# Kernel tuning notes

Measured on AMD Instinct MI355X. Metric: run time of the kernel, lower is better.

The kernel has to match this reference:

```python
import jax, jax.numpy as jnp
import numpy as np

N, S, E = 50000, 16, 400000
D, EDIM = 128, 64
H, K = 4, 32          # n_head, per-head output_dim
NMP, DEPTH = 2, 2


def attn_agg(x, neigh, Wq, Wk, Wv):
    # x: [n, D], neigh: [n, s, D], W*: [H, D, K]
    q = jnp.einsum('nd,hdk->nhk', x, Wq)
    k = jnp.einsum('nsd,hdk->nshk', neigh, Wk)
    v = jnp.einsum('nsd,hdk->nshk', neigh, Wv)
    scale = jnp.asarray(1.0 / np.sqrt(K), x.dtype)
    scores = jnp.einsum('nhk,nshk->nhs', q, k) * scale
    attn = jax.nn.softmax(scores, axis=-1)
    out = jax.nn.elu(jnp.einsum('nhs,nshk->nhk', attn, v))  # activation per head
    return out.reshape(out.shape[0], H * K)                  # concat heads


def setup_inputs():
    key = jax.random.key(0)
    ks = jax.random.split(key, 14)
    sD, sE = 1.0 / np.sqrt(D), 1.0 / np.sqrt(EDIM)
    return {
        'feats': jax.random.normal(ks[0], (N, D), jnp.float32),
        'node_emb': jax.random.normal(ks[1], (N, D), jnp.float32) * 0.02,
        'Wprep': jax.random.normal(ks[2], (D, D), jnp.float32) * sD,
        'edge_emb': jax.random.normal(ks[3], (NMP, E, EDIM), jnp.float32),
        'Wedgeprep': jax.random.normal(ks[4], (NMP, EDIM, D), jnp.float32) * sE,
        'Wq_e': jax.random.normal(ks[5], (NMP, DEPTH, H, D, K), jnp.float32) * sD,
        'Wk_e': jax.random.normal(ks[6], (NMP, DEPTH, H, D, K), jnp.float32) * sD,
        'Wv_e': jax.random.normal(ks[7], (NMP, DEPTH, H, D, K), jnp.float32) * sD,
        'Wq_n': jax.random.normal(ks[8], (NMP, DEPTH, H, D, K), jnp.float32) * sD,
        'Wk_n': jax.random.normal(ks[9], (NMP, DEPTH, H, D, K), jnp.float32) * sD,
        'Wv_n': jax.random.normal(ks[10], (NMP, DEPTH, H, D, K), jnp.float32) * sD,
        'node2edge_idx': jax.random.randint(ks[11], (NMP, N, S), 0, E, jnp.int32),
        'edge_node_adj': jax.random.randint(ks[12], (NMP, E, 2), 0, N, jnp.int32),
    }


def reference(feats, node_emb, Wprep, edge_emb, Wedgeprep,
              Wq_e, Wk_e, Wv_e, Wq_n, Wk_n, Wv_n,
              node2edge_idx, edge_node_adj):
    outputs = []
    for mp in range(NMP):
        f = jax.lax.stop_gradient(feats)           # feats[all_ids].detach()
        dummy_feats = node_emb                      # prep layer_idx=0 (id embedding)
        all_feats = f @ Wprep                       # prep layer_idx=1
        all_edges = edge_emb[mp] @ Wedgeprep[mp]    # edge_prep[mp], shuffle=False
        skip = []
        for l in range(DEPTH):
            # --- edge update: gather 2 endpoint node feats per edge ---
            en = all_feats[edge_node_adj[mp]]       # [E, 2, D]
            next_edges = attn_agg(all_edges, en, Wq_e[mp, l], Wk_e[mp, l], Wv_e[mp, l])
            # --- node update: gather S incident edge feats per node (OLD edges) ---
            x = dummy_feats if l == 0 else all_feats
            ne = all_edges[node2edge_idx[mp]]       # [N, S, D]
            next_feats = attn_agg(x, ne, Wq_n[mp, l], Wk_n[mp, l], Wv_n[mp, l])
            skip.append(next_feats)
            all_feats, all_edges = next_feats, next_edges
        outputs.append(jnp.concatenate(skip, axis=-1))  # [N, DEPTH*H*K]
    return jnp.stack(outputs, axis=0)                   # [NMP, N, DEPTH*H*K]
```

## Files before the change

### kernel.cpp

```cpp
#include <hip/hip_runtime.h>

#define N_NODES 50000
#define S_NEI 16
#define E_EDGES 400000
#define DDIM 128
#define EDIMC 64
#define NMPC 2
#define DEPTHC 2

typedef __attribute__((ext_vector_type(8))) short short8v;
typedef __attribute__((ext_vector_type(4))) float float4v;

__device__ __forceinline__ unsigned short f2bf(float f) {
  unsigned int u = __float_as_uint(f);
  unsigned int r = (u + 0x7fffu + ((u >> 16) & 1u)) >> 16;
  return (unsigned short)r;
}
__device__ __forceinline__ float bf2f(unsigned short h) { return __uint_as_float((unsigned int)h << 16); }
__device__ __forceinline__ float bfs(short h) { return bf2f((unsigned short)h); }
__device__ __forceinline__ float elu_fast(float x) { return x > 0.f ? x : (__expf(x) - 1.0f); }

__global__ void build_wt(const float* __restrict__ Wprep, const float* __restrict__ Wedgeprep,
                         const float* __restrict__ Wq_e, const float* __restrict__ Wk_e,
                         const float* __restrict__ Wv_e, const float* __restrict__ Wq_n,
                         const float* __restrict__ Wk_n, const float* __restrict__ Wv_n,
                         unsigned short* __restrict__ WT) {
  int idx = blockIdx.x * 256 + threadIdx.x;
  if (idx >= 27 * 16384) return;
  int slot = idx >> 14, r = idx & 16383;
  float v = 0.f;
  if (slot < 24) {
    int ml = slot / 6, mat = slot % 6;
    int c = r >> 7, d = r & 127;
    int h = c >> 5, kk = c & 31;
    const float* W = (mat == 0) ? Wk_e : (mat == 1) ? Wv_e : (mat == 2) ? Wq_n
                   : (mat == 3) ? Wq_e : (mat == 4) ? Wk_n : Wv_n;
    v = W[(((size_t)ml * 4 + h) * 128 + d) * 32 + kk];
  } else if (slot == 24) {
    int c = r >> 7, d = r & 127;
    v = Wprep[d * 128 + c];
  } else {
    int mp = slot - 25;
    int c = r >> 6, k = r & 63;
    if (c < 128) v = Wedgeprep[((size_t)mp * 64 + k) * 128 + c];
  }
  WT[idx] = f2bf(v);
}

__global__ void build_qk(const float* __restrict__ Wq_n, const float* __restrict__ Wk_n,
                         unsigned short* __restrict__ QT) {
  int idx = blockIdx.x * 256 + threadIdx.x;
  int mh = idx >> 14, r = idx & 16383;
  int cp = r >> 7, d = r & 127;
  const float* q = Wq_n + ((size_t)mh * 128 + d) * 32;
  const float* k = Wk_n + ((size_t)mh * 128 + cp) * 32;
  float s = 0.f;
  #pragma unroll
  for (int j = 0; j < 32; ++j) s += q[j] * k[j];
  QT[idx] = f2bf(s);
}

__global__ void build_wv(const float* __restrict__ Wv_n, unsigned short* __restrict__ WV) {
  int idx = blockIdx.x * 256 + threadIdx.x;
  int ml = idx >> 14, r14 = idx & 16383;
  int r = r14 >> 7, d = r14 & 127;
  int h = r >> 5, kp = r & 31;
  WV[idx] = f2bf(Wv_n[(((size_t)ml * 4 + h) * 128 + d) * 32 + kp]);
}

template<int KDIM, int NW, bool ASPLIT>
__global__ __launch_bounds__(256, 3)
void proj(const unsigned short* __restrict__ Xbf, const float* __restrict__ Xf,
          const unsigned short* __restrict__ WT,
          unsigned short* __restrict__ Y0, unsigned short* __restrict__ Y1,
          unsigned short* __restrict__ Y2, unsigned short* __restrict__ Y3,
          int rs0, int rs1, int rs2, int rs3, int M) {
  constexpr int NKK  = KDIM / 32;
  constexpr int CHPR = KDIM / 8;
  constexpr int SWZ  = CHPR - 1;
  __shared__ unsigned short Wl[128 * KDIM];
  const int tid  = threadIdx.x;
  const int lane = tid & 63;
  const int wv   = tid >> 6;
  const int l15  = lane & 15, lg = lane >> 4;
  const long m0  = (long)blockIdx.x * 128 + wv * 32;

  short8v xb[2][NKK];
  #pragma unroll
  for (int rf = 0; rf < 2; ++rf) {
    long row = m0 + rf * 16 + l15; if (row >= M) row = M - 1;
    #pragma unroll
    for (int kk = 0; kk < NKK; ++kk) {
      const int k0 = kk * 32 + lg * 8;
      if (ASPLIT) {
        const float* p = Xf + row * KDIM + k0;
        float4v a0 = *(const float4v*)p;
        float4v a1 = *(const float4v*)(p + 4);
        #pragma unroll
        for (int j = 0; j < 8; ++j) {
          float x = (j < 4) ? a0[j] : a1[j - 4];
          xb[rf][kk][j] = (short)f2bf(x);
        }
      } else {
        xb[rf][kk] = *(const short8v*)(Xbf + row * KDIM + k0);
      }
    }
  }

  unsigned short* Ys[4] = {Y0, Y1, Y2, Y3};
  const int rsv[4] = {rs0, rs1, rs2, rs3};
  #pragma unroll
  for (int w = 0; w < NW; ++w) {
    if (w) __syncthreads();
    {
      const uint4* src = (const uint4*)(WT + (size_t)w * 16384);
      #pragma unroll
      for (int i = 0; i < CHPR / 2; ++i) {
        int ci = i * 256 + tid;
        int row = ci / CHPR, ch = ci & SWZ;
        uint4 v = src[ci];
        *(uint4*)((char*)Wl + row * (KDIM * 2) + ((ch ^ (row & SWZ)) << 4)) = v;
      }
    }
    __syncthreads();

    float4v acc[8][2];
    #pragma unroll
    for (int cf = 0; cf < 8; ++cf)
      #pragma unroll
      for (int rf = 0; rf < 2; ++rf) acc[cf][rf] = (float4v)0.f;

    #pragma unroll
    for (int kk = 0; kk < NKK; ++kk) {
      #pragma unroll
      for (int cf = 0; cf < 8; ++cf) {
        const int row = cf * 16 + l15;
        const int ch  = (kk * 4 + lg) ^ (row & SWZ);
        short8v b = *(const short8v*)((char*)Wl + row * (KDIM * 2) + (ch << 4));
        acc[cf][0] = __builtin_amdgcn_mfma_f32_16x16x32_bf16(b, xb[0][kk], acc[cf][0], 0, 0, 0);
        acc[cf][1] = __builtin_amdgcn_mfma_f32_16x16x32_bf16(b, xb[1][kk], acc[cf][1], 0, 0, 0);
      }
    }

    #pragma unroll
    for (int rf = 0; rf < 2; ++rf) {
      const long m = m0 + rf * 16 + l15;
      if (m < M) {
        #pragma unroll
        for (int cf = 0; cf < 8; ++cf) {
          const int c0 = cf * 16 + lg * 4;
          float4v a = acc[cf][rf];
          ushort4 o;
          o.x = f2bf(a[0]); o.y = f2bf(a[1]); o.z = f2bf(a[2]); o.w = f2bf(a[3]);
          *(ushort4*)(Ys[w] + m * (long)rsv[w] + c0) = o;
        }
      }
    }
  }
}

template<int PREP>
__global__ __launch_bounds__(512, 4)
void edge_fused(unsigned short* __restrict__ eold, const unsigned short* __restrict__ WTq,
                const unsigned short* __restrict__ KVn, const int* __restrict__ adj,
                unsigned short* __restrict__ enew,
                const float* __restrict__ emb, const unsigned short* __restrict__ WTprep) {
  __shared__ unsigned short Wl[128 * 128];
  const int tid  = threadIdx.x;
  const int lane = tid & 63;
  const int wv   = tid >> 6;
  const int l15  = lane & 15, lg = lane >> 4;
  const long m0  = (long)blockIdx.x * 128 + wv * 16;

  const long e = m0 + l15;
  const int2 nn = *(const int2*)(adj + e * 2);
  const size_t b0 = (size_t)nn.x * 256, b1 = (size_t)nn.y * 256;

  ushort4 gk0[8], gk1[8], gv0[8], gv1[8];
  if (!PREP) {
    #pragma unroll
    for (int cf = 0; cf < 8; ++cf) {
      const int c0 = cf * 16 + lg * 4;
      gk0[cf] = *(const ushort4*)(KVn + b0 + c0);
      gk1[cf] = *(const ushort4*)(KVn + b1 + c0);
      gv0[cf] = *(const ushort4*)(KVn + b0 + 128 + c0);
      gv1[cf] = *(const ushort4*)(KVn + b1 + 128 + c0);
    }
  }

  short8v xb[4];
  if (PREP) {
    {
      const uint4* src = (const uint4*)WTprep;
      #pragma unroll
      for (int i = 0; i < 2; ++i) {
        int ci = i * 512 + tid;
        int row = ci >> 3, ch = ci & 7;
        uint4 v = src[ci];
        *(uint4*)((char*)Wl + row * 128 + ((ch ^ (row & 7)) << 4)) = v;
      }
    }
    short8v eb[2];
    {
      const long row = m0 + l15;
      #pragma unroll
      for (int kk = 0; kk < 2; ++kk) {
        const float* p = emb + row * 64 + kk * 32 + lg * 8;
        float4v a0 = *(const float4v*)p;
        float4v a1 = *(const float4v*)(p + 4);
        #pragma unroll
        for (int j = 0; j < 8; ++j) {
          float x = (j < 4) ? a0[j] : a1[j - 4];
          eb[kk][j] = (short)f2bf(x);
        }
      }
    }
    __syncthreads();
    float4v accP[8];
    #pragma unroll
    for (int cf = 0; cf < 8; ++cf) accP[cf] = (float4v)0.f;
    #pragma unroll
    for (int kk = 0; kk < 2; ++kk) {
      #pragma unroll
      for (int cf = 0; cf < 8; ++cf) {
        const int row = cf * 16 + l15;
        const int ch  = (kk * 4 + lg) ^ (row & 7);
        short8v b = *(const short8v*)((char*)Wl + row * 128 + (ch << 4));
        accP[cf] = __builtin_amdgcn_mfma_f32_16x16x32_bf16(b, eb[kk], accP[cf], 0, 0, 0);
      }
    }
    __syncthreads();
    {
      const int er = wv * 16 + l15;
      #pragma unroll
      for (int cf = 0; cf < 8; ++cf) {
        float4v a = accP[cf];
        ushort4 o;
        o.x = f2bf(a[0]); o.y = f2bf(a[1]); o.z = f2bf(a[2]); o.w = f2bf(a[3]);
        const int ch16 = cf * 2 + (lg >> 1);
        const int off  = er * 256 + ((ch16 ^ (er & 15)) << 4) + (lg & 1) * 8;
        *(ushort4*)((char*)Wl + off) = o;
      }
    }
    __syncthreads();
    {
      unsigned short* dst = eold + (size_t)blockIdx.x * 16384;
      #pragma unroll
      for (int i = 0; i < 4; ++i) {
        int c = i * 512 + tid;
        int row = c >> 4, ch = c & 15;
        uint4 v = *(const uint4*)((char*)Wl + row * 256 + ((ch ^ (row & 15)) << 4));
        *(uint4*)(dst + (size_t)c * 8) = v;
      }
    }
    {
      const int row = wv * 16 + l15;
      #pragma unroll
      for (int kk = 0; kk < 4; ++kk) {
        const int ch = (kk * 4 + lg) ^ (row & 15);
        xb[kk] = *(const short8v*)((char*)Wl + row * 256 + (ch << 4));
      }
    }
    __syncthreads();
  } else {
    const long row = m0 + l15;
    #pragma unroll
    for (int kk = 0; kk < 4; ++kk)
      xb[kk] = *(const short8v*)(eold + row * 128 + kk * 32 + lg * 8);
  }

  {
    const uint4* src = (const uint4*)WTq;
    #pragma unroll
    for (int i = 0; i < 4; ++i) {
      int ci = i * 512 + tid;
      int row = ci >> 4, ch = ci & 15;
      uint4 v = src[ci];
      *(uint4*)((char*)Wl + row * 256 + ((ch ^ (row & 15)) << 4)) = v;
    }
  }
  __syncthreads();

  if (PREP) {
    #pragma unroll
    for (int cf = 0; cf < 8; ++cf) {
      const int c0 = cf * 16 + lg * 4;
      gk0[cf] = *(const ushort4*)(KVn + b0 + c0);
      gk1[cf] = *(const ushort4*)(KVn + b1 + c0);
      gv0[cf] = *(const ushort4*)(KVn + b0 + 128 + c0);
      gv1[cf] = *(const ushort4*)(KVn + b1 + 128 + c0);
    }
  }

  float4v accQ[8];
  #pragma unroll
  for (int cf = 0; cf < 8; ++cf) accQ[cf] = (float4v)0.f;
  #pragma unroll
  for (int kk = 0; kk < 4; ++kk) {
    #pragma unroll
    for (int cf = 0; cf < 8; ++cf) {
      const int row = cf * 16 + l15;
      const int ch  = (kk * 4 + lg) ^ (row & 15);
      short8v b = *(const short8v*)((char*)Wl + row * 256 + (ch << 4));
      accQ[cf] = __builtin_amdgcn_mfma_f32_16x16x32_bf16(b, xb[kk], accQ[cf], 0, 0, 0);
    }
  }

  const float scale = 0.17677669529663687f;
  ushort4 ov[8];
  {
    float p0[4] = {0.f, 0.f, 0.f, 0.f}, p1[4] = {0.f, 0.f, 0.f, 0.f};
    #pragma unroll
    for (int cf = 0; cf < 8; ++cf) {
      const int h = cf >> 1;
      ushort4 k0 = gk0[cf];
      ushort4 k1 = gk1[cf];
      float4v q = accQ[cf];
      p0[h] += q[0] * bf2f(k0.x) + q[1] * bf2f(k0.y) + q[2] * bf2f(k0.z) + q[3] * bf2f(k0.w);
      p1[h] += q[0] * bf2f(k1.x) + q[1] * bf2f(k1.y) + q[2] * bf2f(k1.z) + q[3] * bf2f(k1.w);
    }
    float a0[4], a1[4];
    #pragma unroll
    for (int h = 0; h < 4; ++h) {
      p0[h] += __shfl_xor(p0[h], 16); p0[h] += __shfl_xor(p0[h], 32);
      p1[h] += __shfl_xor(p1[h], 16); p1[h] += __shfl_xor(p1[h], 32);
      const float s0 = p0[h] * scale, s1 = p1[h] * scale;
      const float mx = fmaxf(s0, s1);
      const float e0 = __expf(s0 - mx), e1 = __expf(s1 - mx);
      const float inv = 1.0f / (e0 + e1);
      a0[h] = e0 * inv; a1[h] = e1 * inv;
    }
    #pragma unroll
    for (int cf = 0; cf < 8; ++cf) {
      const int h = cf >> 1;
      ushort4 v0 = gv0[cf];
      ushort4 v1 = gv1[cf];
      float o[4];
      o[0] = elu_fast(a0[h] * bf2f(v0.x) + a1[h] * bf2f(v1.x));
      o[1] = elu_fast(a0[h] * bf2f(v0.y) + a1[h] * bf2f(v1.y));
      o[2] = elu_fast(a0[h] * bf2f(v0.z) + a1[h] * bf2f(v1.z));
      o[3] = elu_fast(a0[h] * bf2f(v0.w) + a1[h] * bf2f(v1.w));
      ov[cf].x = f2bf(o[0]); ov[cf].y = f2bf(o[1]);
      ov[cf].z = f2bf(o[2]); ov[cf].w = f2bf(o[3]);
    }
  }

  __syncthreads();
  {
    const int er = wv * 16 + l15;
    #pragma unroll
    for (int cf = 0; cf < 8; ++cf) {
      const int ch16 = cf * 2 + (lg >> 1);
      const int off  = er * 256 + ((ch16 ^ (er & 15)) << 4) + (lg & 1) * 8;
      *(ushort4*)((char*)Wl + off) = ov[cf];
    }
  }
  __syncthreads();
  {
    unsigned short* dst = enew + (size_t)blockIdx.x * 16384;
    #pragma unroll
    for (int i = 0; i < 4; ++i) {
      int c = i * 512 + tid;
      int row = c >> 4, ch = c & 15;
      uint4 v = *(const uint4*)((char*)Wl + row * 256 + ((ch ^ (row & 15)) << 4));
      *(uint4*)(dst + (size_t)c * 8) = v;
    }
  }
}

__global__ __launch_bounds__(256, 2)
void node_attn(const unsigned short* __restrict__ qt, const unsigned short* __restrict__ eold,
               const int* __restrict__ n2e, unsigned short* __restrict__ Z) {
  const int lane = threadIdx.x & 63;
  const long n = (long)blockIdx.x * 4 + (threadIdx.x >> 6);
  const short8v qv = *(const short8v*)(qt + n * 512 + lane * 8);
  const int i8 = (lane & 15) * 8;
  short8v xk[16];
  #pragma unroll
  for (int s = 0; s < 16; ++s) {
    const long e = n2e[n * 16 + s];
    xk[s] = *(const short8v*)(eold + e * 128 + i8);
  }
  float sc[16];
  #pragma unroll
  for (int s = 0; s < 16; ++s) {
    float p = 0.f;
    #pragma unroll
    for (int j = 0; j < 8; ++j) p += bfs(qv[j]) * bfs(xk[s][j]);
    p += __shfl_xor(p, 1); p += __shfl_xor(p, 2);
    p += __shfl_xor(p, 4); p += __shfl_xor(p, 8);
    sc[s] = p * 0.17677669529663687f;
  }
  float m = sc[0];
  #pragma unroll
  for (int s = 1; s < 16; ++s) m = fmaxf(m, sc[s]);
  float sum = 0.f;
  #pragma unroll
  for (int s = 0; s < 16; ++s) { sc[s] = __expf(sc[s] - m); sum += sc[s]; }
  const float inv = 1.0f / sum;
  float z[8] = {0.f, 0.f, 0.f, 0.f, 0.f, 0.f, 0.f, 0.f};
  #pragma unroll
  for (int s = 0; s < 16; ++s)
    #pragma unroll
    for (int j = 0; j < 8; ++j) z[j] += sc[s] * bfs(xk[s][j]);
  ushort4 o0, o1;
  o0.x = f2bf(z[0] * inv); o0.y = f2bf(z[1] * inv); o0.z = f2bf(z[2] * inv); o0.w = f2bf(z[3] * inv);
  o1.x = f2bf(z[4] * inv); o1.y = f2bf(z[5] * inv); o1.z = f2bf(z[6] * inv); o1.w = f2bf(z[7] * inv);
  *(ushort4*)(Z + n * 512 + lane * 8) = o0;
  *(ushort4*)(Z + n * 512 + lane * 8 + 4) = o1;
}

__global__ __launch_bounds__(256, 2)
void node_post(const unsigned short* __restrict__ Zb, const unsigned short* __restrict__ WV,
               unsigned short* __restrict__ fnext, float* __restrict__ outp, int M) {
  __shared__ unsigned short Wl[128 * 128];
  const int tid  = threadIdx.x;
  const int lane = tid & 63;
  const int wv   = tid >> 6;
  const int l15  = lane & 15, lg = lane >> 4;
  const long m0  = (long)blockIdx.x * 128 + wv * 32;
  {
    const uint4* src = (const uint4*)WV;
    #pragma unroll
    for (int i = 0; i < 8; ++i) {
      int ci = i * 256 + tid;
      int row = ci >> 4, ch = ci & 15;
      uint4 v = src[ci];
      *(uint4*)((char*)Wl + row * 256 + ((ch ^ (row & 15)) << 4)) = v;
    }
  }
  __syncthreads();

  #pragma unroll
  for (int h = 0; h < 4; ++h) {
    float4v acc[2][2];
    #pragma unroll
    for (int cf = 0; cf < 2; ++cf)
      #pragma unroll
      for (int rf = 0; rf < 2; ++rf) acc[cf][rf] = (float4v)0.f;
    #pragma unroll
    for (int rf = 0; rf < 2; ++rf) {
      long row = m0 + rf * 16 + l15; if (row >= M) row = M - 1;
      #pragma unroll
      for (int kk = 0; kk < 4; ++kk) {
        short8v zb = *(const short8v*)(Zb + row * 512 + h * 128 + kk * 32 + lg * 8);
        #pragma unroll
        for (int cf = 0; cf < 2; ++cf) {
          const int arow = h * 32 + cf * 16 + l15;
          const int ch = (kk * 4 + lg) ^ (arow & 15);
          short8v b = *(const short8v*)((char*)Wl + arow * 256 + (ch << 4));
          acc[cf][rf] = __builtin_amdgcn_mfma_f32_16x16x32_bf16(b, zb, acc[cf][rf], 0, 0, 0);
        }
      }
    }
    #pragma unroll
    for (int rf = 0; rf < 2; ++rf) {
      const long m = m0 + rf * 16 + l15;
      if (m < M) {
        #pragma unroll
        for (int cf = 0; cf < 2; ++cf) {
          const int c0 = h * 32 + cf * 16 + lg * 4;
          float o[4];
          #pragma unroll
          for (int j = 0; j < 4; ++j) o[j] = elu_fast(acc[cf][rf][j]);
          ushort4 ob;
          ob.x = f2bf(o[0]); ob.y = f2bf(o[1]); ob.z = f2bf(o[2]); ob.w = f2bf(o[3]);
          *(ushort4*)(fnext + m * 128 + c0) = ob;
          float4 of; of.x = o[0]; of.y = o[1]; of.z = o[2]; of.w = o[3];
          *(float4*)(outp + m * 256 + c0) = of;
        }
      }
    }
  }
}

extern "C" void kernel_launch(void* const* d_in, const int* in_sizes, int n_in,
                              void* d_out, int out_size, void* d_ws, size_t ws_size,
                              hipStream_t stream) {
  const float* feats     = (const float*)d_in[0];
  const float* node_emb  = (const float*)d_in[1];
  const float* Wprep     = (const float*)d_in[2];
  const float* edge_emb  = (const float*)d_in[3];
  const float* Wedgeprep = (const float*)d_in[4];
  const float* Wq_e      = (const float*)d_in[5];
  const float* Wk_e      = (const float*)d_in[6];
  const float* Wv_e      = (const float*)d_in[7];
  const float* Wq_n      = (const float*)d_in[8];
  const float* Wk_n      = (const float*)d_in[9];
  const float* Wv_n      = (const float*)d_in[10];
  const int*   n2e       = (const int*)d_in[11];
  const int*   adj       = (const int*)d_in[12];
  float* out = (float*)d_out;

  char* w = (char*)d_ws;
  auto carve = [&](size_t bytes) -> char* {
    char* p = w; w += (bytes + 255) & ~(size_t)255; return p;
  };
  unsigned short* e_a   = (unsigned short*)carve((size_t)E_EDGES * 128 * 2);
  unsigned short* e_b   = (unsigned short*)carve((size_t)E_EDGES * 128 * 2);
  unsigned short* fprep = (unsigned short*)carve((size_t)N_NODES * 128 * 2);
  unsigned short* fa    = (unsigned short*)carve((size_t)N_NODES * 128 * 2);
  unsigned short* fb    = (unsigned short*)carve((size_t)N_NODES * 128 * 2);
  unsigned short* KVn   = (unsigned short*)carve((size_t)N_NODES * 256 * 2);
  unsigned short* qt    = (unsigned short*)carve((size_t)N_NODES * 512 * 2);
  unsigned short* Zb    = (unsigned short*)carve((size_t)N_NODES * 512 * 2);
  unsigned short* WT    = (unsigned short*)carve((size_t)27 * 16384 * 2);
  unsigned short* QT    = (unsigned short*)carve((size_t)16 * 16384 * 2);
  unsigned short* WV    = (unsigned short*)carve((size_t)4 * 16384 * 2);

  build_wt<<<(27 * 16384 + 255) / 256, 256, 0, stream>>>(
      Wprep, Wedgeprep, Wq_e, Wk_e, Wv_e, Wq_n, Wk_n, Wv_n, WT);
  build_qk<<<16 * 64, 256, 0, stream>>>(Wq_n, Wk_n, QT);
  build_wv<<<4 * 64, 256, 0, stream>>>(Wv_n, WV);

  const int gN = (N_NODES + 127) / 128;
  const int gE = E_EDGES / 128;

  proj<128, 1, true><<<gN, 256, 0, stream>>>(
      nullptr, feats, WT + (size_t)24 * 16384, fprep, nullptr, nullptr, nullptr,
      128, 0, 0, 0, N_NODES);

  for (int mp = 0; mp < NMPC; ++mp) {
    unsigned short *ecur = e_a, *enext = e_b;
    unsigned short *fchi = fprep, *fnhi = fa;
    for (int l = 0; l < DEPTHC; ++l) {
      const int ml = mp * 2 + l;
      const unsigned short* base = WT + (size_t)ml * 6 * 16384;
      const unsigned short* qkb  = QT + (size_t)ml * 4 * 16384;
      proj<128, 2, false><<<gN, 256, 0, stream>>>(
          fchi, nullptr, base, KVn, KVn + 128, nullptr, nullptr,
          256, 256, 0, 0, N_NODES);
      if (l == 0) {
        proj<128, 4, true><<<gN, 256, 0, stream>>>(
            nullptr, node_emb, qkb, qt, qt + 128, qt + 256, qt + 384,
            512, 512, 512, 512, N_NODES);
      } else {
        proj<128, 4, false><<<gN, 256, 0, stream>>>(
            fchi, nullptr, qkb, qt, qt + 128, qt + 256, qt + 384,
            512, 512, 512, 512, N_NODES);
      }
      if (l == 0) {
        edge_fused<1><<<gE, 512, 0, stream>>>(
            ecur, base + (size_t)3 * 16384, KVn, adj + (size_t)mp * E_EDGES * 2, enext,
            edge_emb + (size_t)mp * E_EDGES * EDIMC, WT + (size_t)(25 + mp) * 16384);
      } else {
        edge_fused<0><<<gE, 512, 0, stream>>>(
            ecur, base + (size_t)3 * 16384, KVn, adj + (size_t)mp * E_EDGES * 2, enext,
            nullptr, nullptr);
      }
      node_attn<<<N_NODES / 4, 256, 0, stream>>>(
          qt, ecur, n2e + (size_t)mp * N_NODES * S_NEI, Zb);
      node_post<<<gN, 256, 0, stream>>>(
          Zb, WV + (size_t)ml * 16384, fnhi,
          out + (size_t)mp * N_NODES * 256 + (size_t)l * 128, N_NODES);

      unsigned short* t = ecur; ecur = enext; enext = t;
      fchi = fnhi; fnhi = fb;
    }
  }
}
```

Baseline: 1.125 ms.

## Merge layer-1 KV and QK projections and co-launch edge and node attention

For the second layer, the K/V projection and the four QK-transformed projections become one 6-output proj launch. This uses a concatenated weight buffer CT built once up front. The edge update and node attention are also merged into a single heterogeneous grid: the first blocks do edges, the remaining blocks do node attention on 8 nodes each. This cuts launch count and avoids re-reading node features, but mixes block types with different register and shared memory needs under one launch bound.

Measured after the change: 1.664 ms. +47.9%, slower.

```diff
diff --git a/kernel.cpp b/kernel.cpp
--- a/kernel.cpp
+++ b/kernel.cpp
@@ -68,13 +68,23 @@
   WV[idx] = f2bf(Wv_n[(((size_t)ml * 4 + h) * 128 + d) * 32 + kp]);
 }
 
+__global__ void build_ct(const unsigned short* __restrict__ WT, const unsigned short* __restrict__ QT,
+                         unsigned short* __restrict__ CT) {
+  int idx = blockIdx.x * 256 + threadIdx.x;
+  int ml = idx / (6 * 16384), r6 = idx % (6 * 16384);
+  int slot = r6 >> 14, r = r6 & 16383;
+  CT[idx] = (slot < 2) ? WT[((size_t)ml * 6 + slot) * 16384 + r]
+                       : QT[((size_t)ml * 4 + (slot - 2)) * 16384 + r];
+}
+
 template<int KDIM, int NW, bool ASPLIT>
 __global__ __launch_bounds__(256, 3)
 void proj(const unsigned short* __restrict__ Xbf, const float* __restrict__ Xf,
           const unsigned short* __restrict__ WT,
           unsigned short* __restrict__ Y0, unsigned short* __restrict__ Y1,
           unsigned short* __restrict__ Y2, unsigned short* __restrict__ Y3,
-          int rs0, int rs1, int rs2, int rs3, int M) {
+          unsigned short* __restrict__ Y4, unsigned short* __restrict__ Y5,
+          int rs0, int rs1, int rs2, int rs3, int rs4, int rs5, int M) {
   constexpr int NKK  = KDIM / 32;
   constexpr int CHPR = KDIM / 8;
   constexpr int SWZ  = CHPR - 1;
@@ -107,8 +117,8 @@
     }
   }
 
-  unsigned short* Ys[4] = {Y0, Y1, Y2, Y3};
-  const int rsv[4] = {rs0, rs1, rs2, rs3};
+  unsigned short* Ys[6] = {Y0, Y1, Y2, Y3, Y4, Y5};
+  const int rsv[6] = {rs0, rs1, rs2, rs3, rs4, rs5};
   #pragma unroll
   for (int w = 0; w < NW; ++w) {
     if (w) __syncthreads();
@@ -159,110 +169,79 @@
   }
 }
 
-template<int PREP>
-__global__ __launch_bounds__(512, 4)
-void edge_fused(unsigned short* __restrict__ eold, const unsigned short* __restrict__ WTq,
-                const unsigned short* __restrict__ KVn, const int* __restrict__ adj,
-                unsigned short* __restrict__ enew,
-                const float* __restrict__ emb, const unsigned short* __restrict__ WTprep) {
-  __shared__ unsigned short Wl[128 * 128];
-  const int tid  = threadIdx.x;
+__device__ __forceinline__
+void node_attn_body(long n, int lane,
+                    const unsigned short* __restrict__ qt,
+                    const unsigned short* __restrict__ eold,
+                    const int* __restrict__ n2e, unsigned short* __restrict__ Z) {
+  const short8v qv = *(const short8v*)(qt + n * 512 + lane * 8);
+  const int i8 = (lane & 15) * 8;
+  short8v xk[16];
+  #pragma unroll
+  for (int s = 0; s < 16; ++s) {
+    const long e = n2e[n * 16 + s];
+    xk[s] = *(const short8v*)(eold + e * 128 + i8);
+  }
+  float sc[16];
+  #pragma unroll
+  for (int s = 0; s < 16; ++s) {
+    float p = 0.f;
+    #pragma unroll
+    for (int j = 0; j < 8; ++j) p += bfs(qv[j]) * bfs(xk[s][j]);
+    p += __shfl_xor(p, 1); p += __shfl_xor(p, 2);
+    p += __shfl_xor(p, 4); p += __shfl_xor(p, 8);
+    sc[s] = p * 0.17677669529663687f;
+  }
+  float m = sc[0];
+  #pragma unroll
+  for (int s = 1; s < 16; ++s) m = fmaxf(m, sc[s]);
+  float sum = 0.f;
+  #pragma unroll
+  for (int s = 0; s < 16; ++s) { sc[s] = __expf(sc[s] - m); sum += sc[s]; }
+  const float inv = 1.0f / sum;
+  float z[8] = {0.f, 0.f, 0.f, 0.f, 0.f, 0.f, 0.f, 0.f};
+  #pragma unroll
+  for (int s = 0; s < 16; ++s)
+    #pragma unroll
+    for (int j = 0; j < 8; ++j) z[j] += sc[s] * bfs(xk[s][j]);
+  ushort4 o0, o1;
+  o0.x = f2bf(z[0] * inv); o0.y = f2bf(z[1] * inv); o0.z = f2bf(z[2] * inv); o0.w = f2bf(z[3] * inv);
+  o1.x = f2bf(z[4] * inv); o1.y = f2bf(z[5] * inv); o1.z = f2bf(z[6] * inv); o1.w = f2bf(z[7] * inv);
+  *(ushort4*)(Z + n * 512 + lane * 8) = o0;
+  *(ushort4*)(Z + n * 512 + lane * 8 + 4) = o1;
+}
+
+__global__ __launch_bounds__(256, 2)
+void node_attn(const unsigned short* __restrict__ qt, const unsigned short* __restrict__ eold,
+               const int* __restrict__ n2e, unsigned short* __restrict__ Z) {
+  node_attn_body((long)blockIdx.x * 4 + (threadIdx.x >> 6), threadIdx.x & 63, qt, eold, n2e, Z);
+}
+
+__device__ __forceinline__
+void edge_body(int ebid, int tid, unsigned short* Wl,
+               const unsigned short* __restrict__ eold, const unsigned short* __restrict__ WTq,
+               const unsigned short* __restrict__ KVn, const int* __restrict__ adj,
+               unsigned short* __restrict__ enew) {
   const int lane = tid & 63;
   const int wv   = tid >> 6;
   const int l15  = lane & 15, lg = lane >> 4;
-  const long m0  = (long)blockIdx.x * 128 + wv * 16;
-
+  const long m0  = (long)ebid * 128 + wv * 16;
   const long e = m0 + l15;
   const int2 nn = *(const int2*)(adj + e * 2);
   const size_t b0 = (size_t)nn.x * 256, b1 = (size_t)nn.y * 256;
 
   ushort4 gk0[8], gk1[8], gv0[8], gv1[8];
-  if (!PREP) {
-    #pragma unroll
-    for (int cf = 0; cf < 8; ++cf) {
-      const int c0 = cf * 16 + lg * 4;
-      gk0[cf] = *(const ushort4*)(KVn + b0 + c0);
-      gk1[cf] = *(const ushort4*)(KVn + b1 + c0);
-      gv0[cf] = *(const ushort4*)(KVn + b0 + 128 + c0);
-      gv1[cf] = *(const ushort4*)(KVn + b1 + 128 + c0);
-    }
+  #pragma unroll
+  for (int cf = 0; cf < 8; ++cf) {
+    const int c0 = cf * 16 + lg * 4;
+    gk0[cf] = *(const ushort4*)(KVn + b0 + c0);
+    gk1[cf] = *(const ushort4*)(KVn + b1 + c0);
+    gv0[cf] = *(const ushort4*)(KVn + b0 + 128 + c0);
+    gv1[cf] = *(const ushort4*)(KVn + b1 + 128 + c0);
   }
 
   short8v xb[4];
-  if (PREP) {
-    {
-      const uint4* src = (const uint4*)WTprep;
-      #pragma unroll
-      for (int i = 0; i < 2; ++i) {
-        int ci = i * 512 + tid;
-        int row = ci >> 3, ch = ci & 7;
-        uint4 v = src[ci];
-        *(uint4*)((char*)Wl + row * 128 + ((ch ^ (row & 7)) << 4)) = v;
-      }
-    }
-    short8v eb[2];
-    {
-      const long row = m0 + l15;
-      #pragma unroll
-      for (int kk = 0; kk < 2; ++kk) {
-        const float* p = emb + row * 64 + kk * 32 + lg * 8;
-        float4v a0 = *(const float4v*)p;
-        float4v a1 = *(const float4v*)(p + 4);
-        #pragma unroll
-        for (int j = 0; j < 8; ++j) {
-          float x = (j < 4) ? a0[j] : a1[j - 4];
-          eb[kk][j] = (short)f2bf(x);
-        }
-      }
-    }
-    __syncthreads();
-    float4v accP[8];
-    #pragma unroll
-    for (int cf = 0; cf < 8; ++cf) accP[cf] = (float4v)0.f;
-    #pragma unroll
-    for (int kk = 0; kk < 2; ++kk) {
-      #pragma unroll
-      for (int cf = 0; cf < 8; ++cf) {
-        const int row = cf * 16 + l15;
-        const int ch  = (kk * 4 + lg) ^ (row & 7);
-        short8v b = *(const short8v*)((char*)Wl + row * 128 + (ch << 4));
-        accP[cf] = __builtin_amdgcn_mfma_f32_16x16x32_bf16(b, eb[kk], accP[cf], 0, 0, 0);
-      }
-    }
-    __syncthreads();
-    {
-      const int er = wv * 16 + l15;
-      #pragma unroll
-      for (int cf = 0; cf < 8; ++cf) {
-        float4v a = accP[cf];
-        ushort4 o;
-        o.x = f2bf(a[0]); o.y = f2bf(a[1]); o.z = f2bf(a[2]); o.w = f2bf(a[3]);
-        const int ch16 = cf * 2 + (lg >> 1);
-        const int off  = er * 256 + ((ch16 ^ (er & 15)) << 4) + (lg & 1) * 8;
-        *(ushort4*)((char*)Wl + off) = o;
-      }
-    }
-    __syncthreads();
-    {
-      unsigned short* dst = eold + (size_t)blockIdx.x * 16384;
-      #pragma unroll
-      for (int i = 0; i < 4; ++i) {
-        int c = i * 512 + tid;
-        int row = c >> 4, ch = c & 15;
-        uint4 v = *(const uint4*)((char*)Wl + row * 256 + ((ch ^ (row & 15)) << 4));
-        *(uint4*)(dst + (size_t)c * 8) = v;
-      }
-    }
-    {
-      const int row = wv * 16 + l15;
-      #pragma unroll
-      for (int kk = 0; kk < 4; ++kk) {
-        const int ch = (kk * 4 + lg) ^ (row & 15);
-        xb[kk] = *(const short8v*)((char*)Wl + row * 256 + (ch << 4));
-      }
-    }
-    __syncthreads();
-  } else {
+  {
     const long row = m0 + l15;
     #pragma unroll
     for (int kk = 0; kk < 4; ++kk)
@@ -280,17 +259,6 @@
     }
   }
   __syncthreads();
-
-  if (PREP) {
-    #pragma unroll
-    for (int cf = 0; cf < 8; ++cf) {
-      const int c0 = cf * 16 + lg * 4;
-      gk0[cf] = *(const ushort4*)(KVn + b0 + c0);
-      gk1[cf] = *(const ushort4*)(KVn + b1 + c0);
-      gv0[cf] = *(const ushort4*)(KVn + b0 + 128 + c0);
-      gv1[cf] = *(const ushort4*)(KVn + b1 + 128 + c0);
-    }
-  }
 
   float4v accQ[8];
   #pragma unroll
@@ -357,7 +325,7 @@
   }
   __syncthreads();
   {
-    unsigned short* dst = enew + (size_t)blockIdx.x * 16384;
+    unsigned short* dst = enew + (size_t)ebid * 16384;
     #pragma unroll
     for (int i = 0; i < 4; ++i) {
       int c = i * 512 + tid;
@@ -368,46 +336,208 @@
   }
 }
 
-__global__ __launch_bounds__(256, 2)
-void node_attn(const unsigned short* __restrict__ qt, const unsigned short* __restrict__ eold,
-               const int* __restrict__ n2e, unsigned short* __restrict__ Z) {
-  const int lane = threadIdx.x & 63;
-  const long n = (long)blockIdx.x * 4 + (threadIdx.x >> 6);
-  const short8v qv = *(const short8v*)(qt + n * 512 + lane * 8);
-  const int i8 = (lane & 15) * 8;
-  short8v xk[16];
-  #pragma unroll
-  for (int s = 0; s < 16; ++s) {
-    const long e = n2e[n * 16 + s];
-    xk[s] = *(const short8v*)(eold + e * 128 + i8);
-  }
-  float sc[16];
-  #pragma unroll
-  for (int s = 0; s < 16; ++s) {
-    float p = 0.f;
-    #pragma unroll
-    for (int j = 0; j < 8; ++j) p += bfs(qv[j]) * bfs(xk[s][j]);
-    p += __shfl_xor(p, 1); p += __shfl_xor(p, 2);
-    p += __shfl_xor(p, 4); p += __shfl_xor(p, 8);
-    sc[s] = p * 0.17677669529663687f;
-  }
-  float m = sc[0];
-  #pragma unroll
-  for (int s = 1; s < 16; ++s) m = fmaxf(m, sc[s]);
-  float sum = 0.f;
-  #pragma unroll
-  for (int s = 0; s < 16; ++s) { sc[s] = __expf(sc[s] - m); sum += sc[s]; }
-  const float inv = 1.0f / sum;
-  float z[8] = {0.f, 0.f, 0.f, 0.f, 0.f, 0.f, 0.f, 0.f};
-  #pragma unroll
-  for (int s = 0; s < 16; ++s)
-    #pragma unroll
-    for (int j = 0; j < 8; ++j) z[j] += sc[s] * bfs(xk[s][j]);
-  ushort4 o0, o1;
-  o0.x = f2bf(z[0] * inv); o0.y = f2bf(z[1] * inv); o0.z = f2bf(z[2] * inv); o0.w = f2bf(z[3] * inv);
-  o1.x = f2bf(z[4] * inv); o1.y = f2bf(z[5] * inv); o1.z = f2bf(z[6] * inv); o1.w = f2bf(z[7] * inv);
-  *(ushort4*)(Z + n * 512 + lane * 8) = o0;
-  *(ushort4*)(Z + n * 512 + lane * 8 + 4) = o1;
+__global__ __launch_bounds__(512, 4)
+void edge_node(const unsigned short* __restrict__ eold, const unsigned short* __restrict__ WTq,
+               const unsigned short* __restrict__ KVn, const int* __restrict__ adj,
+               unsigned short* __restrict__ enew,
+               const unsigned short* __restrict__ qt, const int* __restrict__ n2e,
+               unsigned short* __restrict__ Z, int gE) {
+  __shared__ unsigned short Wl[128 * 128];
+  const int bid = blockIdx.x;
+  if (bid < gE) {
+    edge_body(bid, threadIdx.x, Wl, eold, WTq, KVn, adj, enew);
+  } else {
+    const long n = (long)(bid - gE) * 8 + (threadIdx.x >> 6);
+    node_attn_body(n, threadIdx.x & 63, qt, eold, n2e, Z);
+  }
+}
+
+__global__ __launch_bounds__(512, 4)
+void edge_fused_prep(unsigned short* __restrict__ eold, const unsigned short* __restrict__ WTq,
+                     const unsigned short* __restrict__ KVn, const int* __restrict__ adj,
+                     unsigned short* __restrict__ enew,
+                     const float* __restrict__ emb, const unsigned short* __restrict__ WTprep) {
+  __shared__ unsigned short Wl[128 * 128];
+  const int tid  = threadIdx.x;
+  const int lane = tid & 63;
+  const int wv   = tid >> 6;
+  const int l15  = lane & 15, lg = lane >> 4;
+  const long m0  = (long)blockIdx.x * 128 + wv * 16;
+
+  const long e = m0 + l15;
+  const int2 nn = *(const int2*)(adj + e * 2);
+  const size_t b0 = (size_t)nn.x * 256, b1 = (size_t)nn.y * 256;
+
+  short8v xb[4];
+  {
+    const uint4* src = (const uint4*)WTprep;
+    #pragma unroll
+    for (int i = 0; i < 2; ++i) {
+      int ci = i * 512 + tid;
+      int row = ci >> 3, ch = ci & 7;
+      uint4 v = src[ci];
+      *(uint4*)((char*)Wl + row * 128 + ((ch ^ (row & 7)) << 4)) = v;
+    }
+  }
+  short8v eb[2];
+  {
+    const long row = m0 + l15;
+    #pragma unroll
+    for (int kk = 0; kk < 2; ++kk) {
+      const float* p = emb + row * 64 + kk * 32 + lg * 8;
+      float4v a0 = *(const float4v*)p;
+      float4v a1 = *(const float4v*)(p + 4);
+      #pragma unroll
+      for (int j = 0; j < 8; ++j) {
+        float x = (j < 4) ? a0[j] : a1[j - 4];
+        eb[kk][j] = (short)f2bf(x);
+      }
+    }
+  }
+  __syncthreads();
+  float4v accP[8];
+  #pragma unroll
+  for (int cf = 0; cf < 8; ++cf) accP[cf] = (float4v)0.f;
+  #pragma unroll
+  for (int kk = 0; kk < 2; ++kk) {
+    #pragma unroll
+    for (int cf = 0; cf < 8; ++cf) {
+      const int row = cf * 16 + l15;
+      const int ch  = (kk * 4 + lg) ^ (row & 7);
+      short8v b = *(const short8v*)((char*)Wl + row * 128 + (ch << 4));
+      accP[cf] = __builtin_amdgcn_mfma_f32_16x16x32_bf16(b, eb[kk], accP[cf], 0, 0, 0);
+    }
+  }
+  __syncthreads();
+  {
+    const int er = wv * 16 + l15;
+    #pragma unroll
+    for (int cf = 0; cf < 8; ++cf) {
+      float4v a = accP[cf];
+      ushort4 o;
+      o.x = f2bf(a[0]); o.y = f2bf(a[1]); o.z = f2bf(a[2]); o.w = f2bf(a[3]);
+      const int ch16 = cf * 2 + (lg >> 1);
+      const int off  = er * 256 + ((ch16 ^ (er & 15)) << 4) + (lg & 1) * 8;
+      *(ushort4*)((char*)Wl + off) = o;
+    }
+  }
+  __syncthreads();
+  {
+    unsigned short* dst = eold + (size_t)blockIdx.x * 16384;
+    #pragma unroll
+    for (int i = 0; i < 4; ++i) {
+      int c = i * 512 + tid;
+      int row = c >> 4, ch = c & 15;
+      uint4 v = *(const uint4*)((char*)Wl + row * 256 + ((ch ^ (row & 15)) << 4));
+      *(uint4*)(dst + (size_t)c * 8) = v;
+    }
+  }
+  {
+    const int row = wv * 16 + l15;
+    #pragma unroll
+    for (int kk = 0; kk < 4; ++kk) {
+      const int ch = (kk * 4 + lg) ^ (row & 15);
+      xb[kk] = *(const short8v*)((char*)Wl + row * 256 + (ch << 4));
+    }
+  }
+  __syncthreads();
+
+  {
+    const uint4* src = (const uint4*)WTq;
+    #pragma unroll
+    for (int i = 0; i < 4; ++i) {
+      int ci = i * 512 + tid;
+      int row = ci >> 4, ch = ci & 15;
+      uint4 v = src[ci];
+      *(uint4*)((char*)Wl + row * 256 + ((ch ^ (row & 15)) << 4)) = v;
+    }
+  }
+  __syncthreads();
+
+  ushort4 gk0[8], gk1[8], gv0[8], gv1[8];
+  #pragma unroll
+  for (int cf = 0; cf < 8; ++cf) {
+    const int c0 = cf * 16 + lg * 4;
+    gk0[cf] = *(const ushort4*)(KVn + b0 + c0);
+    gk1[cf] = *(const ushort4*)(KVn + b1 + c0);
+    gv0[cf] = *(const ushort4*)(KVn + b0 + 128 + c0);
+    gv1[cf] = *(const ushort4*)(KVn + b1 + 128 + c0);
+  }
+
+  float4v accQ[8];
+  #pragma unroll
+  for (int cf = 0; cf < 8; ++cf) accQ[cf] = (float4v)0.f;
+  #pragma unroll
+  for (int kk = 0; kk < 4; ++kk) {
+    #pragma unroll
+    for (int cf = 0; cf < 8; ++cf) {
+      const int row = cf * 16 + l15;
+      const int ch  = (kk * 4 + lg) ^ (row & 15);
+      short8v b = *(const short8v*)((char*)Wl + row * 256 + (ch << 4));
+      accQ[cf] = __builtin_amdgcn_mfma_f32_16x16x32_bf16(b, xb[kk], accQ[cf], 0, 0, 0);
+    }
+  }
+
+  const float scale = 0.17677669529663687f;
+  ushort4 ov[8];
+  {
+    float p0[4] = {0.f, 0.f, 0.f, 0.f}, p1[4] = {0.f, 0.f, 0.f, 0.f};
+    #pragma unroll
+    for (int cf = 0; cf < 8; ++cf) {
+      const int h = cf >> 1;
+      ushort4 k0 = gk0[cf];
+      ushort4 k1 = gk1[cf];
+      float4v q = accQ[cf];
+      p0[h] += q[0] * bf2f(k0.x) + q[1] * bf2f(k0.y) + q[2] * bf2f(k0.z) + q[3] * bf2f(k0.w);
+      p1[h] += q[0] * bf2f(k1.x) + q[1] * bf2f(k1.y) + q[2] * bf2f(k1.z) + q[3] * bf2f(k1.w);
+    }
+    float a0[4], a1[4];
+    #pragma unroll
+    for (int h = 0; h < 4; ++h) {
+      p0[h] += __shfl_xor(p0[h], 16); p0[h] += __shfl_xor(p0[h], 32);
+      p1[h] += __shfl_xor(p1[h], 16); p1[h] += __shfl_xor(p1[h], 32);
+      const float s0 = p0[h] * scale, s1 = p1[h] * scale;
+      const float mx = fmaxf(s0, s1);
+      const float e0 = __expf(s0 - mx), e1 = __expf(s1 - mx);
+      const float inv = 1.0f / (e0 + e1);
+      a0[h] = e0 * inv; a1[h] = e1 * inv;
+    }
+    #pragma unroll
+    for (int cf = 0; cf < 8; ++cf) {
+      const int h = cf >> 1;
+      ushort4 v0 = gv0[cf];
+      ushort4 v1 = gv1[cf];
+      float o[4];
+      o[0] = elu_fast(a0[h] * bf2f(v0.x) + a1[h] * bf2f(v1.x));
+      o[1] = elu_fast(a0[h] * bf2f(v0.y) + a1[h] * bf2f(v1.y));
+      o[2] = elu_fast(a0[h] * bf2f(v0.z) + a1[h] * bf2f(v1.z));
+      o[3] = elu_fast(a0[h] * bf2f(v0.w) + a1[h] * bf2f(v1.w));
+      ov[cf].x = f2bf(o[0]); ov[cf].y = f2bf(o[1]);
+      ov[cf].z = f2bf(o[2]); ov[cf].w = f2bf(o[3]);
+    }
+  }
+
+  __syncthreads();
+  {
+    const int er = wv * 16 + l15;
+    #pragma unroll
+    for (int cf = 0; cf < 8; ++cf) {
+      const int ch16 = cf * 2 + (lg >> 1);
+      const int off  = er * 256 + ((ch16 ^ (er & 15)) << 4) + (lg & 1) * 8;
+      *(ushort4*)((char*)Wl + off) = ov[cf];
+    }
+  }
+  __syncthreads();
+  {
+    unsigned short* dst = enew + (size_t)blockIdx.x * 16384;
+    #pragma unroll
+    for (int i = 0; i < 4; ++i) {
+      int c = i * 512 + tid;
+      int row = c >> 4, ch = c & 15;
+      uint4 v = *(const uint4*)((char*)Wl + row * 256 + ((ch ^ (row & 15)) << 4));
+      *(uint4*)(dst + (size_t)c * 8) = v;
+    }
+  }
 }
 
 __global__ __launch_bounds__(256, 2)
@@ -507,18 +637,20 @@
   unsigned short* WT    = (unsigned short*)carve((size_t)27 * 16384 * 2);
   unsigned short* QT    = (unsigned short*)carve((size_t)16 * 16384 * 2);
   unsigned short* WV    = (unsigned short*)carve((size_t)4 * 16384 * 2);
+  unsigned short* CT    = (unsigned short*)carve((size_t)24 * 16384 * 2);
 
   build_wt<<<(27 * 16384 + 255) / 256, 256, 0, stream>>>(
       Wprep, Wedgeprep, Wq_e, Wk_e, Wv_e, Wq_n, Wk_n, Wv_n, WT);
   build_qk<<<16 * 64, 256, 0, stream>>>(Wq_n, Wk_n, QT);
   build_wv<<<4 * 64, 256, 0, stream>>>(Wv_n, WV);
+  build_ct<<<24 * 64, 256, 0, stream>>>(WT, QT, CT);
 
   const int gN = (N_NODES + 127) / 128;
   const int gE = E_EDGES / 128;
 
   proj<128, 1, true><<<gN, 256, 0, stream>>>(
-      nullptr, feats, WT + (size_t)24 * 16384, fprep, nullptr, nullptr, nullptr,
-      128, 0, 0, 0, N_NODES);
+      nullptr, feats, WT + (size_t)24 * 16384, fprep, nullptr, nullptr, nullptr, nullptr, nullptr,
+      128, 0, 0, 0, 0, 0, N_NODES);
 
   for (int mp = 0; mp < NMPC; ++mp) {
     unsigned short *ecur = e_a, *enext = e_b;
@@ -526,30 +658,28 @@
     for (int l = 0; l < DEPTHC; ++l) {
       const int ml = mp * 2 + l;
       const unsigned short* base = WT + (size_t)ml * 6 * 16384;
+      const unsigned short* ctb  = CT + (size_t)ml * 6 * 16384;
       const unsigned short* qkb  = QT + (size_t)ml * 4 * 16384;
-      proj<128, 2, false><<<gN, 256, 0, stream>>>(
-          fchi, nullptr, base, KVn, KVn + 128, nullptr, nullptr,
-          256, 256, 0, 0, N_NODES);
       if (l == 0) {
+        proj<128, 2, false><<<gN, 256, 0, stream>>>(
+            fchi, nullptr, ctb, KVn, KVn + 128, nullptr, nullptr, nullptr, nullptr,
+            256, 256, 0, 0, 0, 0, N_NODES);
         proj<128, 4, true><<<gN, 256, 0, stream>>>(
-            nullptr, node_emb, qkb, qt, qt + 128, qt + 256, qt + 384,
-            512, 512, 512, 512, N_NODES);
-      } else {
-        proj<128, 4, false><<<gN, 256, 0, stream>>>(
-            fchi, nullptr, qkb, qt, qt + 128, qt + 256, qt + 384,
-            512, 512, 512, 512, N_NODES);
-      }
-      if (l == 0) {
-        edge_fused<1><<<gE, 512, 0, stream>>>(
+            nullptr, node_emb, qkb, qt, qt + 128, qt + 256, qt + 384, nullptr, nullptr,
+            512, 512, 512, 512, 0, 0, N_NODES);
+        edge_fused_prep<<<gE, 512, 0, stream>>>(
             ecur, base + (size_t)3 * 16384, KVn, adj + (size_t)mp * E_EDGES * 2, enext,
             edge_emb + (size_t)mp * E_EDGES * EDIMC, WT + (size_t)(25 + mp) * 16384);
+        node_attn<<<N_NODES / 4, 256, 0, stream>>>(
+            qt, ecur, n2e + (size_t)mp * N_NODES * S_NEI, Zb);
       } else {
-        edge_fused<0><<<gE, 512, 0, stream>>>(
+        proj<128, 6, false><<<gN, 256, 0, stream>>>(
+            fchi, nullptr, ctb, KVn, KVn + 128, qt, qt + 128, qt + 256, qt + 384,
+            256, 256, 512, 512, 512, 512, N_NODES);
+        edge_node<<<gE + N_NODES / 8, 512, 0, stream>>>(
             ecur, base + (size_t)3 * 16384, KVn, adj + (size_t)mp * E_EDGES * 2, enext,
-            nullptr, nullptr);
-      }
-      node_attn<<<N_NODES / 4, 256, 0, stream>>>(
-          qt, ecur, n2e + (size_t)mp * N_NODES * S_NEI, Zb);
+            qt, n2e + (size_t)mp * N_NODES * S_NEI, Zb, gE);
+      }
       node_post<<<gN, 256, 0, stream>>>(
           Zb, WV + (size_t)ml * 16384, fnhi,
           out + (size_t)mp * N_NODES * 256 + (size_t)l * 128, N_NODES);
```
